# Performance work log

Measured on AMD Instinct MI355X. Metric: run time of the kernel, lower is better.

## Reference

```python
import jax, jax.numpy as jnp
import numpy as np

# TT factorization of a 4096 -> 4096 linear layer
IN_SHAPE = (8, 8, 8, 8)    # input_tt_shape, prod = 4096
OUT_SHAPE = (8, 8, 8, 8)   # output_tt_shape, prod = 4096
RANKS = (1, 16, 16, 16, 1) # tt_ranks, len = n_dim + 1
N_DIM = len(IN_SHAPE)
BATCH = 2048
OUT_SIZE = int(np.prod(OUT_SHAPE))
IN_SIZE = int(np.prod(IN_SHAPE))


def setup_inputs() -> dict:
    key = jax.random.key(0)
    ks = jax.random.split(key, N_DIM + 1)
    x = jax.random.normal(ks[0], (BATCH, IN_SIZE), dtype=jnp.float32)
    inp = {"x": x}
    for i in range(N_DIM):
        rows = RANKS[i] * OUT_SHAPE[i]
        cols = IN_SHAPE[i] * RANKS[i + 1]
        # xavier_uniform scale, matching torch init statistics
        limit = float(np.sqrt(6.0 / (rows + cols)))
        inp[f"core{i}"] = jax.random.uniform(
            ks[i + 1], (rows, cols), minval=-limit, maxval=limit, dtype=jnp.float32
        )
    inp["bias"] = jnp.zeros((OUT_SIZE,), dtype=jnp.float32)
    return inp


def reference(x, core0, core1, core2, core3, bias):
    cores = [core0, core1, core2, core3]
    res = x  # [B, prod(IN_SHAPE)]
    # Sequential TT-core contraction, last mode first (faithful to torch loop)
    for k in range(N_DIM - 1, -1, -1):
        res = res.reshape(-1, IN_SHAPE[k])                     # [.., n_k]
        res = res.T                                            # [n_k, ..]
        res = res.reshape(RANKS[k + 1] * IN_SHAPE[k], -1)      # [r_{k+1}*n_k, ..]
        res = cores[k] @ res                                   # [r_k*m_k, ..]
    res = res.reshape(OUT_SIZE, -1).T                          # [B, prod(OUT_SHAPE)]
    return res + bias
```

## Files before the change

### kernel.cpp

```cpp
#include <hip/hip_runtime.h>
#include <hip/hip_bf16.h>
#include <stdint.h>


typedef __bf16 bf16_t;
typedef __bf16 bf16x8 __attribute__((ext_vector_type(8)));
typedef float floatx4 __attribute__((ext_vector_type(4)));

#define BATCH_N 2048
#define KD 4096
#define ND 4096

__device__ static inline void load_lds16(const void* g, void* l) {
    __builtin_amdgcn_global_load_lds(
        (const __attribute__((address_space(1))) void*)g,
        (__attribute__((address_space(3))) void*)l, 16, 0, 0);
}

__global__ __launch_bounds__(256) void prep(const float* __restrict__ x,
                                            const float* __restrict__ c0,
                                            const float* __restrict__ c1,
                                            const float* __restrict__ c2,
                                            const float* __restrict__ c3,
                                            bf16_t* __restrict__ W,
                                            bf16_t* __restrict__ xb) {
    __shared__ float c0s[8 * 16];
    __shared__ float c1s[16 * 8 * 16];
    __shared__ float c2s[16 * 8 * 16];
    __shared__ float c3s[16 * 8];
    __shared__ float Ps[64 * 16];
    __shared__ float T1s[16 * 64];
    const int t = threadIdx.x;

    if (blockIdx.x >= 4096) {
        int g = (blockIdx.x - 4096) * 256 + t;
        const float4* xv = (const float4*)x;
        float4 a = xv[g * 2];
        float4 b = xv[g * 2 + 1];
        bf16x8 o;
        o[0] = (bf16_t)a.x; o[1] = (bf16_t)a.y; o[2] = (bf16_t)a.z; o[3] = (bf16_t)a.w;
        o[4] = (bf16_t)b.x; o[5] = (bf16_t)b.y; o[6] = (bf16_t)b.z; o[7] = (bf16_t)b.w;
        ((bf16x8*)xb)[g] = o;
        return;
    }

    const int b = blockIdx.x;
    const int M23 = b >> 6, N01 = b & 63;
    const int n0 = N01 >> 3, n1 = N01 & 7, m2 = M23 >> 3, m3 = M23 & 7;

    if (t < 128) c0s[t] = c0[(t >> 4) * 128 + n0 * 16 + (t & 15)];
    if (t < 128) c3s[t] = c3[((t >> 3) * 8 + m3) * 8 + (t & 7)];
    for (int i = t; i < 2048; i += 256) {
        int r1 = i >> 7, m1 = (i >> 4) & 7, r2 = i & 15;
        c1s[i] = c1[(r1 * 8 + m1) * 128 + n1 * 16 + r2];
    }
    for (int i = t; i < 2048; i += 256) {
        int r2 = i >> 7, n2 = (i >> 4) & 7, r3 = i & 15;
        c2s[i] = c2[(r2 * 8 + m2) * 128 + n2 * 16 + r3];
    }
    __syncthreads();

    for (int i = t; i < 1024; i += 256) {
        int m01 = i >> 4, r2 = i & 15, m0 = m01 >> 3, m1 = m01 & 7;
        float s = 0.f;
#pragma unroll
        for (int r1 = 0; r1 < 16; ++r1)
            s += c0s[m0 * 16 + r1] * c1s[r1 * 128 + m1 * 16 + r2];
        Ps[i] = s;
    }
    for (int i = t; i < 1024; i += 256) {
        int r2 = i >> 6, n23 = i & 63, n2 = n23 >> 3, n3 = n23 & 7;
        float s = 0.f;
#pragma unroll
        for (int r3 = 0; r3 < 16; ++r3)
            s += c2s[r2 * 128 + n2 * 16 + r3] * c3s[r3 * 8 + n3];
        T1s[i] = s;
    }
    __syncthreads();

    const int n23 = t & 63, q = t >> 6;
#pragma unroll
    for (int g = 0; g < 16; ++g) {
        int m01 = q * 16 + g;
        float s = 0.f;
#pragma unroll
        for (int r2 = 0; r2 < 16; ++r2) s += Ps[m01 * 16 + r2] * T1s[r2 * 64 + n23];
        W[(size_t)(m01 * 64 + M23) * 4096 + N01 * 64 + n23] = (bf16_t)s;
    }
}

__global__ __launch_bounds__(256, 2) void gemm_bt(const bf16_t* __restrict__ A,
                                                  const bf16_t* __restrict__ B,
                                                  const float* __restrict__ bias,
                                                  float* __restrict__ C) {
    __shared__ bf16_t As[128 * 64];
    __shared__ bf16_t Bs[128 * 64];
    const int t = threadIdx.x;
    const int bid = blockIdx.x;
    const int xcd = bid & 7, g8 = bid >> 3;
    const int bm = xcd * 2 + (g8 & 1);
    const int bn = g8 >> 1;
    const int lane = t & 63, wave = t >> 6;
    const int wm = wave >> 1, wn = wave & 1;

    const int srow = lane >> 3;
    const int lc = (lane & 7) ^ srow;
    const bf16_t* Agp = A + (size_t)(bm * 128 + wave * 8 + srow) * KD + lc * 8;
    const bf16_t* Bgp = B + (size_t)(bn * 128 + wave * 8 + srow) * KD + lc * 8;
    bf16_t* AsW = As + wave * 512;
    bf16_t* BsW = Bs + wave * 512;

    floatx4 acc[4][4];
    floatx4 zero = {0.f, 0.f, 0.f, 0.f};
#pragma unroll
    for (int i = 0; i < 4; ++i)
#pragma unroll
        for (int j = 0; j < 4; ++j) acc[i][j] = zero;

    const int fr = lane & 15;
    const int fc = lane >> 4;

    for (int k0 = 0; k0 < KD; k0 += 64) {
        __syncthreads();
#pragma unroll
        for (int j = 0; j < 4; ++j) {
            load_lds16(Agp + (size_t)(j * 32) * KD + k0, AsW + j * 2048);
            load_lds16(Bgp + (size_t)(j * 32) * KD + k0, BsW + j * 2048);
        }
        __syncthreads();

#pragma unroll
        for (int kk = 0; kk < 2; ++kk) {
            const int pA = (fc + kk * 4) ^ (fr & 7);
            bf16x8 af[4], bf[4];
#pragma unroll
            for (int im = 0; im < 4; ++im)
                af[im] = *(const bf16x8*)(As + (wm * 64 + im * 16 + fr) * 64 + pA * 8);
#pragma unroll
            for (int in = 0; in < 4; ++in)
                bf[in] = *(const bf16x8*)(Bs + (wn * 64 + in * 16 + fr) * 64 + pA * 8);
#pragma unroll
            for (int im = 0; im < 4; ++im)
#pragma unroll
                for (int in = 0; in < 4; ++in)
                    acc[im][in] = __builtin_amdgcn_mfma_f32_16x16x32_bf16(
                        af[im], bf[in], acc[im][in], 0, 0, 0);
        }
    }

    const int rl = lane >> 4, cl = lane & 15;
    const size_t rbase = (size_t)bm * 128 + wm * 64;
    const int cbase = bn * 128 + wn * 64;
#pragma unroll
    for (int im = 0; im < 4; ++im) {
#pragma unroll
        for (int in = 0; in < 4; ++in) {
            int col = cbase + in * 16 + cl;
            float bv = bias[col];
#pragma unroll
            for (int r = 0; r < 4; ++r) {
                size_t row = rbase + im * 16 + rl * 4 + r;
                C[row * ND + col] = acc[im][in][r] + bv;
            }
        }
    }
}

extern "C" void kernel_launch(void* const* d_in, const int* in_sizes, int n_in,
                              void* d_out, int out_size, void* d_ws, size_t ws_size,
                              hipStream_t stream) {
    const float* x  = (const float*)d_in[0];
    const float* c0 = (const float*)d_in[1];
    const float* c1 = (const float*)d_in[2];
    const float* c2 = (const float*)d_in[3];
    const float* c3 = (const float*)d_in[4];
    const float* bias = (const float*)d_in[5];
    float* out = (float*)d_out;

    char* ws = (char*)d_ws;
    bf16_t* Xb = (bf16_t*)ws;
    bf16_t* W  = (bf16_t*)(ws + (16u << 20));

    prep<<<8192, 256, 0, stream>>>(x, c0, c1, c2, c3, W, Xb);
    gemm_bt<<<512, 256, 0, stream>>>(Xb, W, bias, out);
}
```

Before: 181.4 us.

## Split TT weight build into partial-core precompute and register-tiled W assembly

The single prep kernel recomputed the c0·c1 and c2·c3 partial products in every one of 4096 blocks. They are now computed once per (n0,n1) and (m2,m3) slice in a first kernel and written to scratch space borrowed from the output buffer. A new build_w kernel then assembles W as a rank-16 contraction, holding T slices in registers and writing packed bf16x4 values. This removes the redundant partial products and shared-memory staging at the cost of an extra launch and a global round-trip for the small intermediates.

```diff
diff --git a/kernel.cpp b/kernel.cpp
--- a/kernel.cpp
+++ b/kernel.cpp
@@ -5,6 +5,7 @@
 
 typedef __bf16 bf16_t;
 typedef __bf16 bf16x8 __attribute__((ext_vector_type(8)));
+typedef __bf16 bf16x4 __attribute__((ext_vector_type(4)));
 typedef float floatx4 __attribute__((ext_vector_type(4)));
 
 #define BATCH_N 2048
@@ -17,75 +18,115 @@
         (__attribute__((address_space(3))) void*)l, 16, 0, 0);
 }
 
-__global__ __launch_bounds__(256) void prep(const float* __restrict__ x,
-                                            const float* __restrict__ c0,
-                                            const float* __restrict__ c1,
-                                            const float* __restrict__ c2,
-                                            const float* __restrict__ c3,
-                                            bf16_t* __restrict__ W,
-                                            bf16_t* __restrict__ xb) {
-    __shared__ float c0s[8 * 16];
-    __shared__ float c1s[16 * 8 * 16];
-    __shared__ float c2s[16 * 8 * 16];
-    __shared__ float c3s[16 * 8];
-    __shared__ float Ps[64 * 16];
-    __shared__ float T1s[16 * 64];
+__global__ __launch_bounds__(256) void prep0(const float* __restrict__ x,
+                                             const float* __restrict__ c0,
+                                             const float* __restrict__ c1,
+                                             const float* __restrict__ c2,
+                                             const float* __restrict__ c3,
+                                             bf16_t* __restrict__ xb,
+                                             float* __restrict__ Pg,
+                                             float* __restrict__ Tg) {
     const int t = threadIdx.x;
-
-    if (blockIdx.x >= 4096) {
-        int g = (blockIdx.x - 4096) * 256 + t;
+    const int b = blockIdx.x;
+
+    if (b < 4096) {
+        int g = b * 256 + t;
         const float4* xv = (const float4*)x;
         float4 a = xv[g * 2];
-        float4 b = xv[g * 2 + 1];
+        float4 c = xv[g * 2 + 1];
         bf16x8 o;
         o[0] = (bf16_t)a.x; o[1] = (bf16_t)a.y; o[2] = (bf16_t)a.z; o[3] = (bf16_t)a.w;
-        o[4] = (bf16_t)b.x; o[5] = (bf16_t)b.y; o[6] = (bf16_t)b.z; o[7] = (bf16_t)b.w;
+        o[4] = (bf16_t)c.x; o[5] = (bf16_t)c.y; o[6] = (bf16_t)c.z; o[7] = (bf16_t)c.w;
         ((bf16x8*)xb)[g] = o;
         return;
     }
 
+    __shared__ float s0[128];
+    __shared__ float s1[2048];
+
+    if (b < 4160) {
+        const int n01 = b - 4096, n0 = n01 >> 3, n1 = n01 & 7;
+        if (t < 128) s0[t] = c0[(t >> 4) * 128 + n0 * 16 + (t & 15)];
+        for (int i = t; i < 2048; i += 256) {
+            int r1 = i >> 7, m1 = (i >> 4) & 7, r2 = i & 15;
+            s1[i] = c1[(r1 * 8 + m1) * 128 + n1 * 16 + r2];
+        }
+        __syncthreads();
+#pragma unroll
+        for (int j = 0; j < 4; ++j) {
+            int o = j * 256 + t, m01 = o >> 4, r2 = o & 15;
+            int m0 = m01 >> 3, m1 = m01 & 7;
+            float s = 0.f;
+#pragma unroll
+            for (int r1 = 0; r1 < 16; ++r1)
+                s += s0[m0 * 16 + r1] * s1[r1 * 128 + m1 * 16 + r2];
+            Pg[n01 * 1024 + o] = s;
+        }
+        return;
+    }
+
+    {
+        const int m23 = b - 4160, m2 = m23 >> 3, m3 = m23 & 7;
+        if (t < 128) s0[t] = c3[((t >> 3) * 8 + m3) * 8 + (t & 7)];
+        for (int i = t; i < 2048; i += 256) {
+            int r2 = i >> 7, n2 = (i >> 4) & 7, r3 = i & 15;
+            s1[i] = c2[(r2 * 8 + m2) * 128 + n2 * 16 + r3];
+        }
+        __syncthreads();
+#pragma unroll
+        for (int j = 0; j < 4; ++j) {
+            int o = j * 256 + t, n23 = o >> 4, r2 = o & 15;
+            int n2 = n23 >> 3, n3 = n23 & 7;
+            float s = 0.f;
+#pragma unroll
+            for (int r3 = 0; r3 < 16; ++r3)
+                s += s1[r2 * 128 + n2 * 16 + r3] * s0[r3 * 8 + n3];
+            Tg[m23 * 1024 + o] = s;
+        }
+    }
+}
+
+__global__ __launch_bounds__(256) void build_w(const float* __restrict__ Pg,
+                                               const float* __restrict__ Tg,
+                                               bf16_t* __restrict__ W) {
+    const int t = threadIdx.x;
     const int b = blockIdx.x;
-    const int M23 = b >> 6, N01 = b & 63;
-    const int n0 = N01 >> 3, n1 = N01 & 7, m2 = M23 >> 3, m3 = M23 & 7;
-
-    if (t < 128) c0s[t] = c0[(t >> 4) * 128 + n0 * 16 + (t & 15)];
-    if (t < 128) c3s[t] = c3[((t >> 3) * 8 + m3) * 8 + (t & 7)];
-    for (int i = t; i < 2048; i += 256) {
-        int r1 = i >> 7, m1 = (i >> 4) & 7, r2 = i & 15;
-        c1s[i] = c1[(r1 * 8 + m1) * 128 + n1 * 16 + r2];
-    }
-    for (int i = t; i < 2048; i += 256) {
-        int r2 = i >> 7, n2 = (i >> 4) & 7, r3 = i & 15;
-        c2s[i] = c2[(r2 * 8 + m2) * 128 + n2 * 16 + r3];
-    }
-    __syncthreads();
-
-    for (int i = t; i < 1024; i += 256) {
-        int m01 = i >> 4, r2 = i & 15, m0 = m01 >> 3, m1 = m01 & 7;
-        float s = 0.f;
-#pragma unroll
-        for (int r1 = 0; r1 < 16; ++r1)
-            s += c0s[m0 * 16 + r1] * c1s[r1 * 128 + m1 * 16 + r2];
-        Ps[i] = s;
-    }
-    for (int i = t; i < 1024; i += 256) {
-        int r2 = i >> 6, n23 = i & 63, n2 = n23 >> 3, n3 = n23 & 7;
-        float s = 0.f;
-#pragma unroll
-        for (int r3 = 0; r3 < 16; ++r3)
-            s += c2s[r2 * 128 + n2 * 16 + r3] * c3s[r3 * 8 + n3];
-        T1s[i] = s;
-    }
-    __syncthreads();
-
-    const int n23 = t & 63, q = t >> 6;
-#pragma unroll
-    for (int g = 0; g < 16; ++g) {
-        int m01 = q * 16 + g;
-        float s = 0.f;
-#pragma unroll
-        for (int r2 = 0; r2 < 16; ++r2) s += Ps[m01 * 16 + r2] * T1s[r2 * 64 + n23];
-        W[(size_t)(m01 * 64 + M23) * 4096 + N01 * 64 + n23] = (bf16_t)s;
+    const int n01 = b & 63, q = b >> 6;
+    const int cg = t & 15;
+    const int mr = t >> 4;
+    const float* Pb = Pg + n01 * 1024 + q * 256;
+
+#pragma unroll 1
+    for (int ms = 0; ms < 4; ++ms) {
+        const int m23 = ms * 16 + mr;
+        float Tr[4][16];
+#pragma unroll
+        for (int jj = 0; jj < 4; ++jj) {
+            const float4* tp = (const float4*)(Tg + (m23 * 64 + cg * 4 + jj) * 16);
+#pragma unroll
+            for (int w = 0; w < 4; ++w) {
+                float4 v = tp[w];
+                Tr[jj][w * 4 + 0] = v.x;
+                Tr[jj][w * 4 + 1] = v.y;
+                Tr[jj][w * 4 + 2] = v.z;
+                Tr[jj][w * 4 + 3] = v.w;
+            }
+        }
+#pragma unroll 4
+        for (int ml = 0; ml < 16; ++ml) {
+            float a0 = 0.f, a1 = 0.f, a2 = 0.f, a3 = 0.f;
+#pragma unroll
+            for (int r2 = 0; r2 < 16; ++r2) {
+                float p = Pb[ml * 16 + r2];
+                a0 += p * Tr[0][r2];
+                a1 += p * Tr[1][r2];
+                a2 += p * Tr[2][r2];
+                a3 += p * Tr[3][r2];
+            }
+            bf16x4 o;
+            o[0] = (bf16_t)a0; o[1] = (bf16_t)a1; o[2] = (bf16_t)a2; o[3] = (bf16_t)a3;
+            *(bf16x4*)(W + (size_t)((q * 16 + ml) * 64 + m23) * 4096 + n01 * 64 + cg * 4) = o;
+        }
     }
 }
 
@@ -181,6 +222,10 @@
     bf16_t* Xb = (bf16_t*)ws;
     bf16_t* W  = (bf16_t*)(ws + (16u << 20));
 
-    prep<<<8192, 256, 0, stream>>>(x, c0, c1, c2, c3, W, Xb);
+    float* Pg = (float*)d_out;
+    float* Tg = Pg + 64 * 1024;
+
+    prep0<<<4224, 256, 0, stream>>>(x, c0, c1, c2, c3, Xb, Pg, Tg);
+    build_w<<<256, 256, 0, stream>>>(Pg, Tg, W);
     gemm_bt<<<512, 256, 0, stream>>>(Xb, W, bias, out);
 }
```

Measured after the change: 177.5 us. 1.02x faster.
